# Optimization experiments

Measured on AMD Instinct MI355X. Metric: run time of the kernel, lower is better.

## Reference

```python
import jax, jax.numpy as jnp
import numpy as np

NF = 64        # num_feat
DG = 16        # deformable_groups
K = 3
KK = K * K
CG = NF // DG  # channels per deformable group


def lrelu(x):
    return jnp.where(x >= 0, x, 0.1 * x)


def conv3x3(x, w, b):
    y = jax.lax.conv_general_dilated(
        x, w, window_strides=(1, 1), padding=((1, 1), (1, 1)),
        dimension_numbers=('NCHW', 'OIHW', 'NCHW'))
    return y + b[None, :, None, None]


def _bilinear(feat, py, px):
    # feat: (C, H, W); py, px: arbitrary shape S -> (C,) + S; zeros outside bounds
    H, W = feat.shape[-2:]
    y0f = jnp.floor(py)
    x0f = jnp.floor(px)
    dy = py - y0f
    dx = px - x0f
    y0 = y0f.astype(jnp.int32)
    x0 = x0f.astype(jnp.int32)
    out = jnp.zeros(feat.shape[:1] + py.shape, feat.dtype)
    for yy, xx, wgt in ((y0, x0, (1 - dy) * (1 - dx)),
                        (y0, x0 + 1, (1 - dy) * dx),
                        (y0 + 1, x0, dy * (1 - dx)),
                        (y0 + 1, x0 + 1, dy * dx)):
        valid = (yy >= 0) & (yy < H) & (xx >= 0) & (xx < W)
        v = feat[:, jnp.clip(yy, 0, H - 1), jnp.clip(xx, 0, W - 1)]
        out = out + v * (wgt * valid)[None]
    return out


def backwarp(x, flow):
    # x: (N,C,H,W); flow: (N,2,H,W) with channels (dx, dy) in pixels
    N, C, H, W = x.shape
    gy, gx = jnp.meshgrid(jnp.arange(H, dtype=x.dtype),
                          jnp.arange(W, dtype=x.dtype), indexing='ij')
    px = gx[None] + flow[:, 0]
    py = gy[None] + flow[:, 1]
    return jax.vmap(_bilinear)(x, py, px)


def dcn_v2(x, offset, mask, w, b):
    # x: (N,C,H,W); offset: (N, DG*KK*2, H, W) as consecutive (dy,dx) pairs;
    # mask: (N, DG*KK, H, W) already sigmoided. stride=1, pad=1, k=3.
    N, C, H, W = x.shape
    off = offset.reshape(N, DG, KK, 2, H, W)
    dy, dx = off[:, :, :, 0], off[:, :, :, 1]            # (N,DG,KK,H,W)
    gy, gx = jnp.meshgrid(jnp.arange(H, dtype=x.dtype),
                          jnp.arange(W, dtype=x.dtype), indexing='ij')
    ky = (jnp.arange(KK) // K - K // 2).astype(x.dtype)  # tap row offset: -1,0,1
    kx = (jnp.arange(KK) % K - K // 2).astype(x.dtype)   # tap col offset
    py = dy + gy[None, None, None] + ky[None, None, :, None, None]
    px = dx + gx[None, None, None] + kx[None, None, :, None, None]
    xg = x.reshape(N, DG, CG, H, W)
    sampled = jax.vmap(jax.vmap(_bilinear))(xg, py, px)  # (N,DG,CG,KK,H,W)
    sampled = sampled * mask.reshape(N, DG, 1, KK, H, W)
    wr = w.reshape(-1, DG, CG, KK)                       # (Cout,DG,CG,KK)
    out = jnp.einsum('ngckhw,ogck->nohw', sampled, wr)
    return out + b[None, :, None, None]


def fgda(nbr_feat, ref_feat, flow, w1, b1, w2, b2, w3, b3, w4, b4, dcn_w, dcn_b):
    warped = backwarp(nbr_feat, flow)
    h = lrelu(conv3x3(jnp.concatenate([warped, ref_feat], axis=1), w1, b1))
    h = lrelu(conv3x3(h, w2, b2))
    h = lrelu(conv3x3(h, w3, b3))
    out = conv3x3(h, w4, b4)                             # (N, DG*27, H, W)
    o1, o2, mask = jnp.split(out, 3, axis=1)
    N, _, H, W = flow.shape
    residual = jnp.concatenate([o1, o2], axis=1).reshape(N, -1, 2, H, W)
    # torch.flip(flow, dims=[1]) -> (flow_y, flow_x), broadcast over all taps
    offset = flow[:, ::-1].reshape(N, 1, 2, H, W) + residual
    offset = offset.reshape(N, -1, H, W)
    mask = jax.nn.sigmoid(mask)
    return lrelu(dcn_v2(nbr_feat, offset, mask, dcn_w, dcn_b))


def setup_inputs():
    key = jax.random.key(0)
    ks = jax.random.split(key, 8)
    N, H, W = 8, 128, 128
    s = 0.05
    return {
        'nbr_feat': jax.random.normal(ks[0], (N, NF, H, W), jnp.float32),
        'ref_feat': jax.random.normal(ks[1], (N, NF, H, W), jnp.float32),
        'flow': jax.random.normal(ks[2], (N, 2, H, W), jnp.float32) * 2.0,
        'w1': jax.random.normal(ks[3], (NF, 2 * NF, 3, 3), jnp.float32) * s,
        'b1': jnp.zeros((NF,), jnp.float32),
        'w2': jax.random.normal(ks[4], (NF, NF, 3, 3), jnp.float32) * s,
        'b2': jnp.zeros((NF,), jnp.float32),
        'w3': jax.random.normal(ks[5], (NF, NF, 3, 3), jnp.float32) * s,
        'b3': jnp.zeros((NF,), jnp.float32),
        'w4': jax.random.normal(ks[6], (DG * 3 * KK, NF, 3, 3), jnp.float32) * s,
        'b4': jnp.zeros((DG * 3 * KK,), jnp.float32),
        'dcn_w': jax.random.normal(ks[7], (NF, NF, 3, 3), jnp.float32) * s,
        'dcn_b': jnp.zeros((NF,), jnp.float32),
    }


def reference(nbr_feat, ref_feat, flow, w1, b1, w2, b2, w3, b3, w4, b4, dcn_w, dcn_b):
    return fgda(nbr_feat, ref_feat, flow, w1, b1, w2, b2, w3, b3, w4, b4, dcn_w, dcn_b)
```

## Files before the change

### kernel.cpp

```cpp
#include <hip/hip_runtime.h>
#include <math.h>

#define H 128
#define W 128
#define NB 8
#define NFC 64

typedef __attribute__((ext_vector_type(8))) short s16x8;
typedef __attribute__((ext_vector_type(4))) short s16x4;
typedef __attribute__((ext_vector_type(4))) float f32x4;
typedef __attribute__((ext_vector_type(4))) int   i32x4;
typedef __attribute__((ext_vector_type(2))) int   i32x2;

__device__ __forceinline__ float b2f(short s) {
    return __uint_as_float(((unsigned)(unsigned short)s) << 16);
}
__device__ __forceinline__ short f2bf(float f) {
    unsigned u = __float_as_uint(f);
    u += 0x7FFF + ((u >> 16) & 1);
    return (short)(u >> 16);
}
__device__ __forceinline__ short f2h(float f) {
    _Float16 h = (_Float16)f;
    return __builtin_bit_cast(short, h);
}
__device__ __forceinline__ float h2f(short s) {
    return (float)__builtin_bit_cast(_Float16, s);
}

__global__ __launch_bounds__(256) void k_wt_all(
    const float* __restrict__ w1, const float* __restrict__ w2,
    const float* __restrict__ w3, const float* __restrict__ w4,
    const float* __restrict__ dcw, short* __restrict__ wp)
{
    int idx = blockIdx.x * 256 + threadIdx.x;
    int u = idx / 576;
    int r = idx - u * 576;
    int t = r >> 6, i = r & 63;
    float v;
    if (u < 128) {
        int o = u & 63, icoff = (u >> 6) << 6;
        v = w1[((size_t)(o * 128) + icoff + i) * 9 + t];
    } else if (u < 192) {
        int o = u - 128;
        v = w2[((size_t)(o * 64) + i) * 9 + t];
    } else if (u < 256) {
        int o = u - 192;
        v = w3[((size_t)(o * 64) + i) * 9 + t];
    } else if (u < 704) {
        int o = u - 256;
        v = (o < 432) ? w4[((size_t)(o * 64) + i) * 9 + t] : 0.f;
    } else {
        int o = u - 704;
        v = dcw[((size_t)(o * 64) + i) * 9 + t];
    }
    wp[idx] = f2bf(v);
}

__global__ __launch_bounds__(256) void k_nhwc2(const float* __restrict__ nbr,
                                               const float* __restrict__ ref,
                                               short* __restrict__ nbrG,
                                               short* __restrict__ refH)
{
    int px = blockIdx.x * 256 + threadIdx.x;
    bool isNbr = (px < 131072);
    const float* src;
    if (isNbr) { src = nbr; }
    else       { src = ref; px -= 131072; }
    int n = px >> 14;
    int sp = px & 16383;
    const float* s = src + (size_t)n * 64 * 16384 + sp;
    unsigned pk[32];
    #pragma unroll
    for (int c = 0; c < 32; ++c) {
        float v0 = s[(size_t)(2 * c) * 16384];
        float v1 = s[(size_t)(2 * c + 1) * 16384];
        pk[c] = (unsigned)(unsigned short)f2bf(v0) |
                ((unsigned)(unsigned short)f2bf(v1) << 16);
    }
    if (isNbr) {
        #pragma unroll
        for (int g = 0; g < 16; ++g) {
            i32x2 t;
            t[0] = pk[2 * g]; t[1] = pk[2 * g + 1];
            *(i32x2*)(nbrG + ((size_t)(n * 16 + g) * 16384 + sp) * 4) = t;
        }
    } else {
        i32x4* d = (i32x4*)(refH + (size_t)(n * 16384 + sp) * 64);
        #pragma unroll
        for (int qq = 0; qq < 8; ++qq) {
            i32x4 t;
            t[0] = pk[4 * qq]; t[1] = pk[4 * qq + 1];
            t[2] = pk[4 * qq + 2]; t[3] = pk[4 * qq + 3];
            d[qq] = t;
        }
    }
}

__global__ __launch_bounds__(256) void k_backwarp(const short* __restrict__ nbrG,
                                                  const float* __restrict__ flow,
                                                  short* __restrict__ warped)
{
    int idx = blockIdx.x * 256 + threadIdx.x;
    int px = idx >> 2, qt = idx & 3;
    int n = px >> 14;
    int x = px & 127, y = (px >> 7) & 127;
    float fx = flow[(size_t)(n * 2 + 0) * 16384 + y * 128 + x];
    float fy = flow[(size_t)(n * 2 + 1) * 16384 + y * 128 + x];
    float pxf = (float)x + fx, pyf = (float)y + fy;
    float x0f = floorf(pxf), y0f = floorf(pyf);
    int x0 = (int)x0f, y0 = (int)y0f;
    float dx = pxf - x0f, dy = pyf - y0f;
    float vy0 = ((unsigned)y0 < 128u) ? 1.f : 0.f;
    float vy1 = ((unsigned)(y0 + 1) < 128u) ? 1.f : 0.f;
    float vx0 = ((unsigned)x0 < 128u) ? 1.f : 0.f;
    float vx1 = ((unsigned)(x0 + 1) < 128u) ? 1.f : 0.f;
    float w00 = (1.f - dy) * (1.f - dx) * vy0 * vx0;
    float w01 = (1.f - dy) * dx * vy0 * vx1;
    float w10 = dy * (1.f - dx) * vy1 * vx0;
    float w11 = dy * dx * vy1 * vx1;
    int y0c = min(max(y0, 0), 127), y1c = min(max(y0 + 1, 0), 127);
    int x0c = min(max(x0, 0), 127), x1c = min(max(x0 + 1, 0), 127);
    int xb = min(max(x0, 0), 126);
    bool s0 = (x0c == xb), s1 = (x1c == xb);

    const short* plbase = nbrG + (size_t)n * 16 * 65536;
    s16x8 r0, r1;
    #pragma unroll
    for (int pg = 0; pg < 4; ++pg) {
        const short* pl = plbase + (size_t)(qt * 4 + pg) * 65536;
        s16x8 p0 = *(const s16x8*)(pl + (y0c * 128 + xb) * 4);
        s16x8 p1 = *(const s16x8*)(pl + (y1c * 128 + xb) * 4);
        #pragma unroll
        for (int cc = 0; cc < 4; ++cc) {
            float v00 = b2f(s0 ? p0[cc] : p0[4 + cc]);
            float v01 = b2f(s1 ? p0[cc] : p0[4 + cc]);
            float v10 = b2f(s0 ? p1[cc] : p1[4 + cc]);
            float v11 = b2f(s1 ? p1[cc] : p1[4 + cc]);
            float v = w00 * v00 + w01 * v01 + w10 * v10 + w11 * v11;
            short res = f2bf(v);
            if (pg < 2) r0[pg * 4 + cc] = res;
            else        r1[(pg - 2) * 4 + cc] = res;
        }
    }
    short* o = warped + (size_t)px * 64 + qt * 16;
    *(s16x8*)o = r0;
    *(s16x8*)(o + 8) = r1;
}

template<int MODE>
__global__ __launch_bounds__(256) void k_conv(
    const short* __restrict__ in, const short* __restrict__ wT,
    const float* __restrict__ bias,
    float* __restrict__ partial, short* __restrict__ outB,
    int* __restrict__ offP, short* __restrict__ maskP,
    const float* __restrict__ flow, int n0)
{
    __shared__ __align__(16) short tileS[180 * 64];
    __shared__ __align__(16) short aS[64 * 64];

    int tid = threadIdx.x;
    int bid = blockIdx.x;
    int og = (MODE == 3) ? blockIdx.y : 0;
    int n  = (MODE == 3) ? (n0 + (bid >> 7)) : (bid >> 7);
    int tl = bid & 127;
    int bx = (tl & 7) << 4;
    int by = (tl >> 3) << 3;
    int ln = tid & 63, wv = tid >> 6;
    int c = ln & 15, q = ln >> 4;

    for (int i = tid; i < 1440; i += 256) {
        int pt = i >> 3, c16 = i & 7;
        int ty = pt / 18, tx = pt - ty * 18;
        int gy = by + ty - 1, gx = bx + tx - 1;
        i32x4 v = {0, 0, 0, 0};
        if ((unsigned)gy < 128u && (unsigned)gx < 128u)
            v = *(const i32x4*)(in + (((size_t)n * 128 + gy) * 128 + gx) * 64 + c16 * 8);
        *(i32x4*)((char*)tileS + pt * 128 + ((c16 ^ (pt & 7)) << 4)) = v;
    }

    const short* wbase = wT + ((MODE == 3) ? (size_t)og * 36864 : 0);
    int aoc = tid >> 3, ac8 = tid & 7;
    i32x4 sa0 = *(const i32x4*)(wbase + (size_t)aoc * 576 + ac8 * 8);
    i32x4 sa1 = *(const i32x4*)(wbase + (size_t)(aoc + 32) * 576 + ac8 * 8);

    f32x4 acc[4][2];
    #pragma unroll
    for (int m = 0; m < 4; ++m) {
        acc[m][0] = (f32x4){0.f, 0.f, 0.f, 0.f};
        acc[m][1] = (f32x4){0.f, 0.f, 0.f, 0.f};
    }

    int p0 = 2 * wv, p1 = 2 * wv + 1;
    int pby0 = (p0 >> 2) << 2, pbx0 = (p0 & 3) << 2;
    int pby1 = (p1 >> 2) << 2, pbx1 = (p1 & 3) << 2;
    int cy = c >> 2, cx = c & 3;

    __syncthreads();

    for (int tap = 0; tap < 9; ++tap) {
        *(i32x4*)((char*)aS + aoc * 128 + ((ac8 ^ (aoc & 7)) << 4)) = sa0;
        *(i32x4*)((char*)aS + (aoc + 32) * 128 + ((ac8 ^ ((aoc + 32) & 7)) << 4)) = sa1;
        if (tap < 8) {
            sa0 = *(const i32x4*)(wbase + (size_t)aoc * 576 + (tap + 1) * 64 + ac8 * 8);
            sa1 = *(const i32x4*)(wbase + (size_t)(aoc + 32) * 576 + (tap + 1) * 64 + ac8 * 8);
        }
        __syncthreads();

        int dty = tap / 3, dtx = tap - dty * 3;
        int pta = (pby0 + cy + dty) * 18 + pbx0 + cx + dtx;
        int ptb = (pby1 + cy + dty) * 18 + pbx1 + cx + dtx;
        #pragma unroll
        for (int ih = 0; ih < 2; ++ih) {
            int slot = ih * 4 + q;
            s16x8 bf0 = *(const s16x8*)((const char*)tileS + pta * 128 + ((slot ^ (pta & 7)) << 4));
            s16x8 bf1 = *(const s16x8*)((const char*)tileS + ptb * 128 + ((slot ^ (ptb & 7)) << 4));
            #pragma unroll
            for (int m = 0; m < 4; ++m) {
                int ocl = m * 16 + c;
                s16x8 a = *(const s16x8*)((const char*)aS + ocl * 128 + ((slot ^ (ocl & 7)) << 4));
                acc[m][0] = __builtin_amdgcn_mfma_f32_16x16x32_bf16(a, bf0, acc[m][0], 0, 0, 0);
                acc[m][1] = __builtin_amdgcn_mfma_f32_16x16x32_bf16(a, bf1, acc[m][1], 0, 0, 0);
            }
        }
        __syncthreads();
    }

    #pragma unroll
    for (int p = 0; p < 2; ++p) {
        int pby = p ? pby1 : pby0;
        int pbx = p ? pbx1 : pbx0;
        int y = by + pby + cy;
        int x = bx + pbx + cx;
        size_t pxi = ((size_t)n * 128 + y) * 128 + x;
        float fy = 0.f, fx2 = 0.f;
        if (MODE == 3) {
            fy  = flow[(size_t)(n * 2 + 1) * 16384 + y * 128 + x];
            fx2 = flow[(size_t)(n * 2 + 0) * 16384 + y * 128 + x];
        }
        #pragma unroll
        for (int m = 0; m < 4; ++m) {
            int o0 = m * 16 + q * 4;
            f32x4 v = acc[m][p];
            if (MODE == 0) {
                *(f32x4*)(partial + pxi * 64 + o0) = v;
            } else if (MODE == 1 || MODE == 2) {
                f32x4 bv = *(const f32x4*)(bias + o0);
                if (MODE == 1) {
                    f32x4 pv = *(const f32x4*)(partial + pxi * 64 + o0);
                    v += pv;
                }
                v += bv;
                s16x4 r;
                #pragma unroll
                for (int j = 0; j < 4; ++j) {
                    float t = v[j];
                    t = t >= 0.f ? t : 0.1f * t;
                    r[j] = f2bf(t);
                }
                *(s16x4*)(outB + pxi * 64 + o0) = r;
            } else {
                int oc4 = og * 64 + o0;
                if (oc4 < 432) {
                    f32x4 bv = *(const f32x4*)(bias + oc4);
                    v += bv;
                    size_t nrel = (size_t)(bid >> 7);
                    int pxl = y * 128 + x;
                    if (oc4 < 288) {
                        int gk0 = oc4 >> 1;
                        int g0 = gk0 / 9, t0 = gk0 - g0 * 9;
                        int gk1 = gk0 + 1;
                        int g1 = gk1 / 9, t1 = gk1 - g1 * 9;
                        unsigned pk0 = (unsigned)(unsigned short)f2h(v[0] + fy) |
                                       ((unsigned)(unsigned short)f2h(v[1] + fx2) << 16);
                        unsigned pk1 = (unsigned)(unsigned short)f2h(v[2] + fy) |
                                       ((unsigned)(unsigned short)f2h(v[3] + fx2) << 16);
                        offP[(((nrel * 9 + t0) * 4 + (g0 >> 2)) * 16384 + (size_t)pxl) * 4 + (g0 & 3)] = (int)pk0;
                        offP[(((nrel * 9 + t1) * 4 + (g1 >> 2)) * 16384 + (size_t)pxl) * 4 + (g1 & 3)] = (int)pk1;
                    } else {
                        int gkb = oc4 - 288;
                        #pragma unroll
                        for (int j = 0; j < 4; ++j) {
                            int gk = gkb + j;
                            int g = gk / 9, t = gk - g * 9;
                            maskP[(((nrel * 9 + t) * 4 + (g >> 2)) * 16384 + (size_t)pxl) * 4 + (g & 3)] =
                                f2h(1.f / (1.f + expf(-v[j])));
                        }
                    }
                }
            }
        }
    }
}

__global__ __launch_bounds__(256) void k_dcn(
    const int* __restrict__ offP, const short* __restrict__ maskP,
    const short* __restrict__ nbrG, const short* __restrict__ dcwT,
    const float* __restrict__ dcb, float* __restrict__ out, int n0)
{
    __shared__ __align__(16) short smp[64 * 64];
    __shared__ __align__(16) short aS[64 * 64];

    int tid = threadIdx.x;
    int bid = blockIdx.x;
    int nrel = bid >> 8;
    int rb = bid & 255;
    int y = rb >> 1;
    int xh = (rb & 1) << 6;
    int n = n0 + nrel;

    int xt = tid & 63;
    int sg = tid >> 6;
    int ln = tid & 63, c = ln & 15, q = ln >> 4;
    int x = xh + xt;
    int pxl = y * 128 + x;

    int aoc = tid >> 3, ac8 = tid & 7;
    i32x4 sa0 = *(const i32x4*)(dcwT + (size_t)aoc * 576 + ac8 * 8);
    i32x4 sa1 = *(const i32x4*)(dcwT + (size_t)(aoc + 32) * 576 + ac8 * 8);

    const short* plg0 = nbrG + (size_t)(n * 16 + sg * 4) * 65536;

    f32x4 acc[4];
    #pragma unroll
    for (int m = 0; m < 4; ++m) acc[m] = (f32x4){0.f, 0.f, 0.f, 0.f};

    int brow = sg * 16 + c;

    for (int tap = 0; tap < 9; ++tap) {
        int dty = tap / 3 - 1, dtx = tap - (tap / 3) * 3 - 1;
        size_t obase = (((size_t)(nrel * 9 + tap) * 4 + sg) * 16384 + pxl) * 4;
        i32x4 dd4 = *(const i32x4*)(offP + obase);
        s16x4 mk4 = *(const s16x4*)(maskP + obase);

        s16x8 r01[2];
        #pragma unroll
        for (int gg = 0; gg < 4; ++gg) {
            float dyv = h2f((short)(dd4[gg] & 0xffff));
            float dxv = h2f((short)(((unsigned)dd4[gg]) >> 16));
            float mk  = h2f(mk4[gg]);
            float sy = (float)(y + dty) + dyv;
            float sx = (float)(x + dtx) + dxv;
            float y0f = floorf(sy), x0f = floorf(sx);
            int y0 = (int)y0f, x0 = (int)x0f;
            float ddy = sy - y0f, ddx = sx - x0f;
            float vy0 = ((unsigned)y0 < 128u) ? 1.f : 0.f;
            float vy1 = ((unsigned)(y0 + 1) < 128u) ? 1.f : 0.f;
            float vx0 = ((unsigned)x0 < 128u) ? 1.f : 0.f;
            float vx1 = ((unsigned)(x0 + 1) < 128u) ? 1.f : 0.f;
            float w00 = (1.f - ddy) * (1.f - ddx) * vy0 * vx0;
            float w01 = (1.f - ddy) * ddx * vy0 * vx1;
            float w10 = ddy * (1.f - ddx) * vy1 * vx0;
            float w11 = ddy * ddx * vy1 * vx1;
            int y0c = min(max(y0, 0), 127), y1c = min(max(y0 + 1, 0), 127);
            int x0c = min(max(x0, 0), 127), x1c = min(max(x0 + 1, 0), 127);
            int xb = min(max(x0, 0), 126);
            bool sel0 = (x0c == xb), sel1 = (x1c == xb);
            const short* plg = plg0 + (size_t)gg * 65536;
            s16x8 pr0 = *(const s16x8*)(plg + (y0c * 128 + xb) * 4);
            s16x8 pr1 = *(const s16x8*)(plg + (y1c * 128 + xb) * 4);
            #pragma unroll
            for (int cc = 0; cc < 4; ++cc) {
                float v00 = b2f(sel0 ? pr0[cc] : pr0[4 + cc]);
                float v01 = b2f(sel1 ? pr0[cc] : pr0[4 + cc]);
                float v10 = b2f(sel0 ? pr1[cc] : pr1[4 + cc]);
                float v11 = b2f(sel1 ? pr1[cc] : pr1[4 + cc]);
                float sv = w00 * v00 + w01 * v01 + w10 * v10 + w11 * v11;
                r01[gg >> 1][(gg & 1) * 4 + cc] = f2bf(sv * mk);
            }
        }
        *(s16x8*)((char*)smp + xt * 128 + (((sg * 2 + 0) ^ (xt & 7)) << 4)) = r01[0];
        *(s16x8*)((char*)smp + xt * 128 + (((sg * 2 + 1) ^ (xt & 7)) << 4)) = r01[1];
        *(i32x4*)((char*)aS + aoc * 128 + ((ac8 ^ (aoc & 7)) << 4)) = sa0;
        *(i32x4*)((char*)aS + (aoc + 32) * 128 + ((ac8 ^ ((aoc + 32) & 7)) << 4)) = sa1;
        if (tap < 8) {
            sa0 = *(const i32x4*)(dcwT + (size_t)aoc * 576 + (tap + 1) * 64 + ac8 * 8);
            sa1 = *(const i32x4*)(dcwT + (size_t)(aoc + 32) * 576 + (tap + 1) * 64 + ac8 * 8);
        }
        __syncthreads();

        #pragma unroll
        for (int ih = 0; ih < 2; ++ih) {
            int slot = ih * 4 + q;
            s16x8 bf = *(const s16x8*)((const char*)smp + brow * 128 + ((slot ^ (brow & 7)) << 4));
            #pragma unroll
            for (int m = 0; m < 4; ++m) {
                int ocl = m * 16 + c;
                s16x8 a = *(const s16x8*)((const char*)aS + ocl * 128 + ((slot ^ (ocl & 7)) << 4));
                acc[m] = __builtin_amdgcn_mfma_f32_16x16x32_bf16(a, bf, acc[m], 0, 0, 0);
            }
        }
        __syncthreads();
    }

    #pragma unroll
    for (int m = 0; m < 4; ++m) {
        int o0 = m * 16 + q * 4;
        f32x4 bv = *(const f32x4*)(dcb + o0);
        f32x4 v = acc[m] + bv;
        int xo = xh + sg * 16 + c;
        #pragma unroll
        for (int j = 0; j < 4; ++j) {
            float t = v[j];
            t = t >= 0.f ? t : 0.1f * t;
            out[((size_t)n * 64 + o0 + j) * 16384 + y * 128 + xo] = t;
        }
    }
}

extern "C" void kernel_launch(void* const* d_in, const int* in_sizes, int n_in,
                              void* d_out, int out_size, void* d_ws, size_t ws_size,
                              hipStream_t stream)
{
    const float* nbr  = (const float*)d_in[0];
    const float* ref  = (const float*)d_in[1];
    const float* flow = (const float*)d_in[2];
    const float* w1   = (const float*)d_in[3];
    const float* b1   = (const float*)d_in[4];
    const float* w2   = (const float*)d_in[5];
    const float* b2   = (const float*)d_in[6];
    const float* w3   = (const float*)d_in[7];
    const float* b3   = (const float*)d_in[8];
    const float* w4   = (const float*)d_in[9];
    const float* b4   = (const float*)d_in[10];
    const float* dcw  = (const float*)d_in[11];
    const float* dcb  = (const float*)d_in[12];
    float* out = (float*)d_out;
    char* ws = (char*)d_ws;

    short* nbrG   = (short*)ws;
    short* wpool  = (short*)(ws + 16777216);
    short* warped = (short*)(ws + 17825792);
    short* refH   = (short*)(ws + 34603008);
    float* h1p    = (float*)(ws + 51380224);
    int*   offP   = (int*)(ws + 17825792);
    short* maskP  = (short*)(ws + 55574528);
    short* h3     = (short*)(ws + 74448896);
    short* h1     = warped;
    short* h2     = refH;

    short* wT1a = wpool;
    short* wT1b = wpool + 36864;
    short* wT2  = wpool + 73728;
    short* wT3  = wpool + 110592;
    short* wT4  = wpool + 147456;
    short* dcwT = wpool + 405504;

    k_wt_all<<<1728, 256, 0, stream>>>(w1, w2, w3, w4, dcw, wpool);
    k_nhwc2<<<1024, 256, 0, stream>>>(nbr, ref, nbrG, refH);
    k_backwarp<<<2048, 256, 0, stream>>>(nbrG, flow, warped);

    k_conv<0><<<1024, 256, 0, stream>>>(warped, wT1a, nullptr, h1p, nullptr, nullptr, nullptr, nullptr, 0);
    k_conv<1><<<1024, 256, 0, stream>>>(refH, wT1b, b1, h1p, h1, nullptr, nullptr, nullptr, 0);
    k_conv<2><<<1024, 256, 0, stream>>>(h1, wT2, b2, nullptr, h2, nullptr, nullptr, nullptr, 0);
    k_conv<2><<<1024, 256, 0, stream>>>(h2, wT3, b3, nullptr, h3, nullptr, nullptr, nullptr, 0);

    for (int n0 = 0; n0 < 8; n0 += 4) {
        dim3 g4(512, 7);
        k_conv<3><<<g4, 256, 0, stream>>>(h3, wT4, b4, nullptr, nullptr, offP, maskP, flow, n0);
        k_dcn<<<1024, 256, 0, stream>>>(offP, maskP, nbrG, dcwT, dcb, out, n0);
    }
}
```

Measured before the change: 353.9 us.

## Enlarge conv spatial tile to 16x16 with four pixel blocks per wave

Each conv block now covers a 16x16 output tile instead of 16x8, so the input halo tile grows to 18x18 and each wave holds four 4x4 pixel blocks (16 accumulators) instead of two. Every weight fragment loaded from LDS now feeds four MFMAs instead of two, and the halo overhead per output pixel shrinks. The cost is fewer blocks (512 or 256 per launch instead of 1024 or 512), more LDS per block and more accumulator registers, which may lower occupancy and leave fewer blocks to spread across the GPU's compute units.

```diff
diff --git a/kernel.cpp b/kernel.cpp
--- a/kernel.cpp
+++ b/kernel.cpp
@@ -156,20 +156,20 @@
     int* __restrict__ offP, short* __restrict__ maskP,
     const float* __restrict__ flow, int n0)
 {
-    __shared__ __align__(16) short tileS[180 * 64];
+    __shared__ __align__(16) short tileS[324 * 64];
     __shared__ __align__(16) short aS[64 * 64];
 
     int tid = threadIdx.x;
     int bid = blockIdx.x;
     int og = (MODE == 3) ? blockIdx.y : 0;
-    int n  = (MODE == 3) ? (n0 + (bid >> 7)) : (bid >> 7);
-    int tl = bid & 127;
+    int n  = (MODE == 3) ? (n0 + (bid >> 6)) : (bid >> 6);
+    int tl = bid & 63;
     int bx = (tl & 7) << 4;
-    int by = (tl >> 3) << 3;
+    int by = (tl >> 3) << 4;
     int ln = tid & 63, wv = tid >> 6;
     int c = ln & 15, q = ln >> 4;
 
-    for (int i = tid; i < 1440; i += 256) {
+    for (int i = tid; i < 2592; i += 256) {
         int pt = i >> 3, c16 = i & 7;
         int ty = pt / 18, tx = pt - ty * 18;
         int gy = by + ty - 1, gx = bx + tx - 1;
@@ -184,16 +184,13 @@
     i32x4 sa0 = *(const i32x4*)(wbase + (size_t)aoc * 576 + ac8 * 8);
     i32x4 sa1 = *(const i32x4*)(wbase + (size_t)(aoc + 32) * 576 + ac8 * 8);
 
-    f32x4 acc[4][2];
-    #pragma unroll
-    for (int m = 0; m < 4; ++m) {
-        acc[m][0] = (f32x4){0.f, 0.f, 0.f, 0.f};
-        acc[m][1] = (f32x4){0.f, 0.f, 0.f, 0.f};
-    }
-
-    int p0 = 2 * wv, p1 = 2 * wv + 1;
-    int pby0 = (p0 >> 2) << 2, pbx0 = (p0 & 3) << 2;
-    int pby1 = (p1 >> 2) << 2, pbx1 = (p1 & 3) << 2;
+    f32x4 acc[4][4];
+    #pragma unroll
+    for (int m = 0; m < 4; ++m)
+        #pragma unroll
+        for (int p = 0; p < 4; ++p)
+            acc[m][p] = (f32x4){0.f, 0.f, 0.f, 0.f};
+
     int cy = c >> 2, cx = c & 3;
 
     __syncthreads();
@@ -208,30 +205,32 @@
         __syncthreads();
 
         int dty = tap / 3, dtx = tap - dty * 3;
-        int pta = (pby0 + cy + dty) * 18 + pbx0 + cx + dtx;
-        int ptb = (pby1 + cy + dty) * 18 + pbx1 + cx + dtx;
+        int ptr0 = (wv * 4 + cy + dty) * 18 + cx + dtx;
         #pragma unroll
         for (int ih = 0; ih < 2; ++ih) {
             int slot = ih * 4 + q;
-            s16x8 bf0 = *(const s16x8*)((const char*)tileS + pta * 128 + ((slot ^ (pta & 7)) << 4));
-            s16x8 bf1 = *(const s16x8*)((const char*)tileS + ptb * 128 + ((slot ^ (ptb & 7)) << 4));
+            s16x8 bf[4];
+            #pragma unroll
+            for (int p = 0; p < 4; ++p) {
+                int ptp = ptr0 + p * 4;
+                bf[p] = *(const s16x8*)((const char*)tileS + ptp * 128 + ((slot ^ (ptp & 7)) << 4));
+            }
             #pragma unroll
             for (int m = 0; m < 4; ++m) {
                 int ocl = m * 16 + c;
                 s16x8 a = *(const s16x8*)((const char*)aS + ocl * 128 + ((slot ^ (ocl & 7)) << 4));
-                acc[m][0] = __builtin_amdgcn_mfma_f32_16x16x32_bf16(a, bf0, acc[m][0], 0, 0, 0);
-                acc[m][1] = __builtin_amdgcn_mfma_f32_16x16x32_bf16(a, bf1, acc[m][1], 0, 0, 0);
+                #pragma unroll
+                for (int p = 0; p < 4; ++p)
+                    acc[m][p] = __builtin_amdgcn_mfma_f32_16x16x32_bf16(a, bf[p], acc[m][p], 0, 0, 0);
             }
         }
         __syncthreads();
     }
 
     #pragma unroll
-    for (int p = 0; p < 2; ++p) {
-        int pby = p ? pby1 : pby0;
-        int pbx = p ? pbx1 : pbx0;
-        int y = by + pby + cy;
-        int x = bx + pbx + cx;
+    for (int p = 0; p < 4; ++p) {
+        int y = by + wv * 4 + cy;
+        int x = bx + p * 4 + cx;
         size_t pxi = ((size_t)n * 128 + y) * 128 + x;
         float fy = 0.f, fx2 = 0.f;
         if (MODE == 3) {
@@ -264,7 +263,7 @@
                 if (oc4 < 432) {
                     f32x4 bv = *(const f32x4*)(bias + oc4);
                     v += bv;
-                    size_t nrel = (size_t)(bid >> 7);
+                    size_t nrel = (size_t)(bid >> 6);
                     int pxl = y * 128 + x;
                     if (oc4 < 288) {
                         int gk0 = oc4 >> 1;
@@ -450,13 +449,13 @@
     k_nhwc2<<<1024, 256, 0, stream>>>(nbr, ref, nbrG, refH);
     k_backwarp<<<2048, 256, 0, stream>>>(nbrG, flow, warped);
 
-    k_conv<0><<<1024, 256, 0, stream>>>(warped, wT1a, nullptr, h1p, nullptr, nullptr, nullptr, nullptr, 0);
-    k_conv<1><<<1024, 256, 0, stream>>>(refH, wT1b, b1, h1p, h1, nullptr, nullptr, nullptr, 0);
-    k_conv<2><<<1024, 256, 0, stream>>>(h1, wT2, b2, nullptr, h2, nullptr, nullptr, nullptr, 0);
-    k_conv<2><<<1024, 256, 0, stream>>>(h2, wT3, b3, nullptr, h3, nullptr, nullptr, nullptr, 0);
+    k_conv<0><<<512, 256, 0, stream>>>(warped, wT1a, nullptr, h1p, nullptr, nullptr, nullptr, nullptr, 0);
+    k_conv<1><<<512, 256, 0, stream>>>(refH, wT1b, b1, h1p, h1, nullptr, nullptr, nullptr, 0);
+    k_conv<2><<<512, 256, 0, stream>>>(h1, wT2, b2, nullptr, h2, nullptr, nullptr, nullptr, 0);
+    k_conv<2><<<512, 256, 0, stream>>>(h2, wT3, b3, nullptr, h3, nullptr, nullptr, nullptr, 0);
 
     for (int n0 = 0; n0 < 8; n0 += 4) {
-        dim3 g4(512, 7);
+        dim3 g4(256, 7);
         k_conv<3><<<g4, 256, 0, stream>>>(h3, wT4, b4, nullptr, nullptr, offP, maskP, flow, n0);
         k_dcn<<<1024, 256, 0, stream>>>(offP, maskP, nbrG, dcwT, dcb, out, n0);
     }
```

Result: slower. 361.1 us (+2.0%).
